# Optimization experiments

Hardware: AMD Instinct MI355X
Metric: run time of the kernel (lower is better)

Reference implementation:

```python
import jax, jax.numpy as jnp
import numpy as np

N, H, W = 128, 64, 64
CH_I, CH_H, CH_Q = 2, 150, 10
N_ACT = 8


def conv3x3(x, w):
    # x: [N,H,W,Cin], w: [3,3,Cin,Cout], 'same' padding, stride 1
    return jax.lax.conv_general_dilated(
        x, w, window_strides=(1, 1), padding='SAME',
        dimension_numbers=('NHWC', 'HWIO', 'NHWC'))


def setup_inputs() -> dict:
    key = jax.random.key(0)
    ks = jax.random.split(key, 9)
    std = 0.01
    x = jax.random.normal(ks[0], (N, H, W, CH_I), dtype=jnp.float32)
    S1 = jax.random.randint(ks[1], (N,), 0, H, dtype=jnp.int32)
    S2 = jax.random.randint(ks[2], (N,), 0, W, dtype=jnp.int32)
    w0 = std * jax.random.normal(ks[3], (3, 3, CH_I, CH_H), dtype=jnp.float32)
    b0 = jnp.zeros((CH_H,), dtype=jnp.float32)
    w_r = std * jax.random.normal(ks[4], (3, 3, CH_H, 1), dtype=jnp.float32)
    w_q = std * jax.random.normal(ks[5], (3, 3, 2, CH_Q), dtype=jnp.float32)
    w_sw = std * jax.random.normal(ks[6], (3, 3, 2, CH_Q), dtype=jnp.float32)
    w_sw2 = std * jax.random.normal(ks[7], (3, 3, 2, CH_Q), dtype=jnp.float32)
    w_dense = std * jax.random.normal(ks[8], (CH_Q, N_ACT), dtype=jnp.float32)
    return {"x": x, "S1": S1, "S2": S2, "VInum": 36,
            "w0": w0, "b0": b0, "w_r": w_r, "w_q": w_q,
            "w_sw": w_sw, "w_sw2": w_sw2, "w_dense": w_dense}


def reference(x, S1, S2, VInum, w0, b0, w_r, w_q, w_sw, w_sw2, w_dense):
    k = int(VInum)
    h = conv3x3(x, w0) + b0                      # [N,H,W,ch_h]
    r = conv3x3(h, w_r)                          # [N,H,W,1] reward map
    v = jnp.zeros_like(r)
    # first VI step uses conv2 weights
    q = conv3x3(jnp.concatenate([r, v], axis=3), w_q)
    v = jnp.max(q, axis=3, keepdims=True)
    # k-1 shared-weight value-iteration steps
    def body(v, _):
        q = conv3x3(jnp.concatenate([r, v], axis=3), w_sw)
        return jnp.max(q, axis=3, keepdims=True), None
    v, _ = jax.lax.scan(body, v, None, length=k - 1)
    # final step with second shared-weight conv
    q = conv3x3(jnp.concatenate([r, v], axis=3), w_sw2)  # [N,H,W,ch_q]
    # attention: gather Q values at state (S1,S2) per batch element
    q_out = q[jnp.arange(q.shape[0]), S1, S2]            # [N,ch_q]
    logits = q_out @ w_dense                             # [N,8]
    prob_actions = jax.nn.softmax(logits, axis=-1)
    return (logits, prob_actions, q, q_out)
```

## Files before the change

### kernel.cpp

```cpp
#include <hip/hip_runtime.h>
#include <math.h>


typedef float v2f __attribute__((ext_vector_type(2)));

static __device__ __forceinline__ v2f splat2(float s) { v2f r; r.x = s; r.y = s; return r; }
static __device__ __forceinline__ v2f pkfma(v2f w, float v, v2f a) {
#if __has_builtin(__builtin_elementwise_fma)
    return __builtin_elementwise_fma(w, splat2(v), a);
#else
    v2f r; r.x = fmaf(w.x, v, a.x); r.y = fmaf(w.y, v, a.y); return r;
#endif
}
static __device__ __forceinline__ v2f pkmax(v2f a, v2f b) {
#if __has_builtin(__builtin_elementwise_max)
    return __builtin_elementwise_max(a, b);
#else
    v2f r; r.x = fmaxf(a.x, b.x); r.y = fmaxf(a.y, b.y); return r;
#endif
}

#define XROW 69
#define VROW 67
#define VSTR (66 * VROW)

__global__ void
__attribute__((amdgpu_flat_work_group_size(512, 512)))
__attribute__((amdgpu_waves_per_eu(2, 2)))
vin_kernel(const float* __restrict__ x,
           const int* __restrict__ S1,
           const int* __restrict__ S2,
           const int* __restrict__ VInum,
           const float* __restrict__ w0,
           const float* __restrict__ b0,
           const float* __restrict__ w_r,
           const float* __restrict__ w_q,
           const float* __restrict__ w_sw,
           const float* __restrict__ w_sw2,
           const float* __restrict__ w_dense,
           float* __restrict__ out) {
    const int b = blockIdx.x;
    const int t = threadIdx.x;

    __shared__ float xs0[68 * XROW];
    __shared__ float xs1[68 * XROW];
    __shared__ float rs[66 * VROW];
    __shared__ float vpool[2 * VSTR];
    __shared__ float wtA[1620];
    __shared__ float Pp[450];
    __shared__ float Bt[90];
    __shared__ float Bv[9];
    __shared__ float W5c[459];
    __shared__ v2f   swv2[45];
    __shared__ float qsel[10];

    for (int i = t; i < 68 * XROW; i += 512) { xs0[i] = 0.f; xs1[i] = 0.f; }
    for (int i = t; i < 66 * VROW; i += 512) rs[i] = 0.f;
    for (int i = t; i < 2 * VSTR; i += 512) vpool[i] = 0.f;
    if (t < 450) Pp[t] = 0.f;
    if (t < 45) {
        int d = t / 5, ap = t - d * 5;
        v2f w; w.x = w_sw[d * 20 + 10 + 2 * ap]; w.y = w_sw[d * 20 + 10 + 2 * ap + 1];
        swv2[t] = w;
    }
    __syncthreads();

    const int row = t >> 3;
    const int cb  = (t & 7) << 3;

    {
        const float* xb = x + (size_t)b * 64 * 64 * 2;
        const float4* xp = (const float4*)(xb + (row * 64 + cb) * 2);
        #pragma unroll
        for (int g = 0; g < 4; ++g) {
            float4 v4 = xp[g];
            int px = cb + g * 2;
            xs0[(row + 2) * XROW + px + 2] = v4.x;
            xs1[(row + 2) * XROW + px + 2] = v4.y;
            xs0[(row + 2) * XROW + px + 3] = v4.z;
            xs1[(row + 2) * XROW + px + 3] = v4.w;
        }
    }
    for (int idx = t; idx < 1620; idx += 512) {
        int entry = idx / 10, ch = idx - entry * 10;
        int d = entry / 18, rem = entry % 18;
        int uu = rem >> 1, ci = rem & 1;
        int c0 = ch * 15;
        const float* wr = w_r + d * 150;
        const float* wp = w0 + (uu * 2 + ci) * 150;
        float s = 0.f;
        for (int c = c0; c < c0 + 15; ++c) s += wr[c] * wp[c];
        wtA[idx] = s;
    }
    if (t < 90) {
        int d = t / 10, ch = t - d * 10, c0 = ch * 15;
        float s = 0.f;
        for (int c = c0; c < c0 + 15; ++c) s += w_r[d * 150 + c] * b0[c];
        Bt[t] = s;
    }
    __syncthreads();
    if (t < 162) {
        float s = 0.f;
        #pragma unroll
        for (int i = 0; i < 10; ++i) s += wtA[t * 10 + i];
        int d = t / 18, rem = t % 18;
        int uu = rem >> 1, ci = rem & 1;
        int dy = d / 3 - 1, dx = d % 3 - 1;
        int uy = uu / 3 - 1, ux = uu % 3 - 1;
        int eidx = (dy + uy + 2) * 5 + (dx + ux + 2);
        Pp[d * 50 + eidx * 2 + ci] = s;
    } else if (t >= 256 && t < 265) {
        int d = t - 256;
        float s = 0.f;
        #pragma unroll
        for (int i = 0; i < 10; ++i) s += Bt[d * 10 + i];
        Bv[d] = s;
    }
    __syncthreads();
    if (t < 459) {
        int cls = t / 51, j = t - cls * 51;
        int cy = cls / 3, cx = cls % 3;
        float s = 0.f;
        #pragma unroll
        for (int d = 0; d < 9; ++d) {
            int dy = d / 3 - 1, dx = d % 3 - 1;
            bool ok = (cy == 0 || (cy == 1 ? dy >= 0 : dy <= 0)) &&
                      (cx == 0 || (cx == 1 ? dx >= 0 : dx <= 0));
            if (ok) s += (j < 50) ? Pp[d * 50 + j] : Bv[d];
        }
        W5c[t] = s;
    }
    __syncthreads();

    {
        int cy = (row == 0) ? 1 : (row == 63) ? 2 : 0;
        #pragma unroll
        for (int p = 0; p < 8; ++p) {
            int xx = cb + p;
            int cx = (xx == 0) ? 1 : (xx == 63) ? 2 : 0;
            const float* Wp = &W5c[(cy * 3 + cx) * 51];
            float acc = Wp[50];
            #pragma unroll
            for (int e = 0; e < 25; ++e) {
                int xi = (row + e / 5) * XROW + (xx + e % 5);
                acc = fmaf(xs0[xi], Wp[e * 2], acc);
                acc = fmaf(xs1[xi], Wp[e * 2 + 1], acc);
            }
            rs[(row + 1) * VROW + (xx + 1)] = acc;
        }
    }
    __syncthreads();

    const int K = VInum[0];

    v2f Rsw2[8][5];
    {
        float rwin[3][10];
        #pragma unroll
        for (int i = 0; i < 3; ++i) {
            const float* rp = &rs[(row + i) * VROW + cb];
            #pragma unroll
            for (int j = 0; j < 10; ++j) rwin[i][j] = rp[j];
        }
        float vmax[8];
        #pragma unroll
        for (int a = 0; a < 10; ++a) {
            #pragma unroll
            for (int p = 0; p < 8; ++p) {
                float accR = 0.f, accQ = 0.f;
                #pragma unroll
                for (int d = 0; d < 9; ++d) {
                    float rv = rwin[d / 3][p + d % 3];
                    accR = fmaf(w_sw[d * 20 + a], rv, accR);
                    accQ = fmaf(w_q[d * 20 + a],  rv, accQ);
                }
                if (a & 1) Rsw2[p][a >> 1].y = accR; else Rsw2[p][a >> 1].x = accR;
                vmax[p] = (a == 0) ? accQ : fmaxf(vmax[p], accQ);
            }
        }
        #pragma unroll
        for (int p = 0; p < 8; ++p)
            vpool[0 * VSTR + (row + 1) * VROW + (cb + p + 1)] = vmax[p];
    }
    __syncthreads();

    int cur = 0;
    for (int it = 0; it < K - 1; ++it) {
        const float* vb = &vpool[cur * VSTR + row * VROW + cb];
        float vwin[3][10];
        #pragma unroll
        for (int i = 0; i < 3; ++i)
            #pragma unroll
            for (int j = 0; j < 10; ++j) vwin[i][j] = vb[i * VROW + j];
        int nxt = cur ^ 1;
        v2f vmax2[8];
        #pragma unroll
        for (int ap = 0; ap < 5; ++ap) {
            v2f acc2[8];
            #pragma unroll
            for (int d = 0; d < 9; ++d) {
                v2f w2 = swv2[d * 5 + ap];
                #pragma unroll
                for (int p = 0; p < 8; ++p) {
                    float vv = vwin[d / 3][p + d % 3];
                    acc2[p] = (d == 0) ? pkfma(w2, vv, Rsw2[p][ap])
                                       : pkfma(w2, vv, acc2[p]);
                }
            }
            #pragma unroll
            for (int p = 0; p < 8; ++p)
                vmax2[p] = (ap == 0) ? acc2[p] : pkmax(vmax2[p], acc2[p]);
        }
        #pragma unroll
        for (int p = 0; p < 8; ++p)
            vpool[nxt * VSTR + (row + 1) * VROW + (cb + p + 1)] =
                fmaxf(vmax2[p].x, vmax2[p].y);
        cur = nxt;
        __syncthreads();
    }

    const int s1 = S1[b], s2 = S2[b];
    {
        float rwin[3][10], vwin[3][10];
        #pragma unroll
        for (int i = 0; i < 3; ++i) {
            const float* rp = &rs[(row + i) * VROW + cb];
            const float* vb = &vpool[cur * VSTR + (row + i) * VROW + cb];
            #pragma unroll
            for (int j = 0; j < 10; ++j) { rwin[i][j] = rp[j]; vwin[i][j] = vb[j]; }
        }
        float qv[8][10];
        #pragma unroll
        for (int a = 0; a < 10; ++a) {
            #pragma unroll
            for (int p = 0; p < 8; ++p) {
                float acc = 0.f;
                #pragma unroll
                for (int d = 0; d < 9; ++d) {
                    acc = fmaf(w_sw2[d * 20 + a],      rwin[d / 3][p + d % 3], acc);
                    acc = fmaf(w_sw2[d * 20 + 10 + a], vwin[d / 3][p + d % 3], acc);
                }
                qv[p][a] = acc;
            }
        }
        {
            float4* qp4 = (float4*)(out + 2048 + ((size_t)((b * 64 + row) * 64 + cb)) * 10);
            #pragma unroll
            for (int g = 0; g < 20; ++g)
                qp4[g] = make_float4(qv[(g * 4) / 10][(g * 4) % 10],
                                     qv[(g * 4 + 1) / 10][(g * 4 + 1) % 10],
                                     qv[(g * 4 + 2) / 10][(g * 4 + 2) % 10],
                                     qv[(g * 4 + 3) / 10][(g * 4 + 3) % 10]);
        }
        if (row == s1) {
            #pragma unroll
            for (int p = 0; p < 8; ++p)
                if (s2 == cb + p) {
                    #pragma unroll
                    for (int a = 0; a < 10; ++a) qsel[a] = qv[p][a];
                }
        }
    }
    __syncthreads();

    if (t == 0) {
        float logits[8];
        float m = -1e30f;
        #pragma unroll
        for (int j = 0; j < 8; ++j) {
            float s = 0.f;
            #pragma unroll
            for (int a = 0; a < 10; ++a) s += qsel[a] * w_dense[a * 8 + j];
            logits[j] = s;
            m = fmaxf(m, s);
        }
        float sum = 0.f;
        float e[8];
        #pragma unroll
        for (int j = 0; j < 8; ++j) { e[j] = expf(logits[j] - m); sum += e[j]; }
        float inv = 1.f / sum;
        #pragma unroll
        for (int j = 0; j < 8; ++j) {
            out[b * 8 + j] = logits[j];
            out[1024 + b * 8 + j] = e[j] * inv;
        }
    }
    if (t < 10) out[5244928 + b * 10 + t] = qsel[t];
}

extern "C" void kernel_launch(void* const* d_in, const int* in_sizes, int n_in,
                              void* d_out, int out_size, void* d_ws, size_t ws_size,
                              hipStream_t stream) {
    const float* x      = (const float*)d_in[0];
    const int*   S1     = (const int*)d_in[1];
    const int*   S2     = (const int*)d_in[2];
    const int*   VInum  = (const int*)d_in[3];
    const float* w0     = (const float*)d_in[4];
    const float* b0     = (const float*)d_in[5];
    const float* w_r    = (const float*)d_in[6];
    const float* w_q    = (const float*)d_in[7];
    const float* w_sw   = (const float*)d_in[8];
    const float* w_sw2  = (const float*)d_in[9];
    const float* w_dense= (const float*)d_in[10];
    float* out = (float*)d_out;

    vin_kernel<<<128, 512, 0, stream>>>(x, S1, S2, VInum, w0, b0, w_r, w_q,
                                        w_sw, w_sw2, w_dense, out);
}
```

Before: 197.1 us.

## Double threads per block, 4 pixels per thread, vectorized LDS window loads

Launches 1024 threads per block instead of 512, so each thread now handles 4 pixels rather than 8. This doubles the waves available to hide LDS latency during the serial value-iteration loop. The shared arrays are padded to 68-float rows so the stencil windows can be read with aligned float4 loads, and each thread keeps its own previous v values in registers rather than reloading them. The packed w_sw weights are now read straight from global memory as uniform loads instead of from LDS. The trade-off is more barrier participants per iteration, a tighter per-thread register budget, and more redundant halo loads per output pixel.

After: 176.7 us. -10.4%, faster.

```diff
diff --git a/kernel.cpp b/kernel.cpp
--- a/kernel.cpp
+++ b/kernel.cpp
@@ -21,12 +21,13 @@
 }
 
 #define XROW 69
-#define VROW 67
-#define VSTR (66 * VROW)
+#define RROW 68
+#define VROW2 68
+#define VSTR2 (66 * VROW2)
 
 __global__ void
-__attribute__((amdgpu_flat_work_group_size(512, 512)))
-__attribute__((amdgpu_waves_per_eu(2, 2)))
+__attribute__((amdgpu_flat_work_group_size(1024, 1024)))
+__attribute__((amdgpu_waves_per_eu(4, 4)))
 vin_kernel(const float* __restrict__ x,
            const int* __restrict__ S1,
            const int* __restrict__ S2,
@@ -44,35 +45,29 @@
 
     __shared__ float xs0[68 * XROW];
     __shared__ float xs1[68 * XROW];
-    __shared__ float rs[66 * VROW];
-    __shared__ float vpool[2 * VSTR];
+    __shared__ float rs[66 * RROW];
+    __shared__ float vpool[2 * VSTR2];
     __shared__ float wtA[1620];
     __shared__ float Pp[450];
     __shared__ float Bt[90];
     __shared__ float Bv[9];
     __shared__ float W5c[459];
-    __shared__ v2f   swv2[45];
     __shared__ float qsel[10];
 
-    for (int i = t; i < 68 * XROW; i += 512) { xs0[i] = 0.f; xs1[i] = 0.f; }
-    for (int i = t; i < 66 * VROW; i += 512) rs[i] = 0.f;
-    for (int i = t; i < 2 * VSTR; i += 512) vpool[i] = 0.f;
+    for (int i = t; i < 68 * XROW; i += 1024) { xs0[i] = 0.f; xs1[i] = 0.f; }
+    for (int i = t; i < 66 * RROW; i += 1024) rs[i] = 0.f;
+    for (int i = t; i < 2 * VSTR2; i += 1024) vpool[i] = 0.f;
     if (t < 450) Pp[t] = 0.f;
-    if (t < 45) {
-        int d = t / 5, ap = t - d * 5;
-        v2f w; w.x = w_sw[d * 20 + 10 + 2 * ap]; w.y = w_sw[d * 20 + 10 + 2 * ap + 1];
-        swv2[t] = w;
-    }
-    __syncthreads();
-
-    const int row = t >> 3;
-    const int cb  = (t & 7) << 3;
+    __syncthreads();
+
+    const int row = t >> 4;
+    const int cb  = (t & 15) << 2;
 
     {
         const float* xb = x + (size_t)b * 64 * 64 * 2;
         const float4* xp = (const float4*)(xb + (row * 64 + cb) * 2);
         #pragma unroll
-        for (int g = 0; g < 4; ++g) {
+        for (int g = 0; g < 2; ++g) {
             float4 v4 = xp[g];
             int px = cb + g * 2;
             xs0[(row + 2) * XROW + px + 2] = v4.x;
@@ -81,7 +76,7 @@
             xs1[(row + 2) * XROW + px + 3] = v4.w;
         }
     }
-    for (int idx = t; idx < 1620; idx += 512) {
+    for (int idx = t; idx < 1620; idx += 1024) {
         int entry = idx / 10, ch = idx - entry * 10;
         int d = entry / 18, rem = entry % 18;
         int uu = rem >> 1, ci = rem & 1;
@@ -135,7 +130,7 @@
     {
         int cy = (row == 0) ? 1 : (row == 63) ? 2 : 0;
         #pragma unroll
-        for (int p = 0; p < 8; ++p) {
+        for (int p = 0; p < 4; ++p) {
             int xx = cb + p;
             int cx = (xx == 0) ? 1 : (xx == 63) ? 2 : 0;
             const float* Wp = &W5c[(cy * 3 + cx) * 51];
@@ -146,27 +141,29 @@
                 acc = fmaf(xs0[xi], Wp[e * 2], acc);
                 acc = fmaf(xs1[xi], Wp[e * 2 + 1], acc);
             }
-            rs[(row + 1) * VROW + (xx + 1)] = acc;
+            rs[(row + 1) * RROW + xx + 2] = acc;
         }
     }
     __syncthreads();
 
     const int K = VInum[0];
 
-    v2f Rsw2[8][5];
+    v2f Rsw2[4][5];
+    float vprev[4];
     {
-        float rwin[3][10];
+        float rwin[3][6];
         #pragma unroll
         for (int i = 0; i < 3; ++i) {
-            const float* rp = &rs[(row + i) * VROW + cb];
-            #pragma unroll
-            for (int j = 0; j < 10; ++j) rwin[i][j] = rp[j];
-        }
-        float vmax[8];
+            const float4* rp = (const float4*)&rs[(row + i) * RROW + cb];
+            float4 cA = rp[0], cB = rp[1];
+            rwin[i][0] = cA.y; rwin[i][1] = cA.z; rwin[i][2] = cA.w;
+            rwin[i][3] = cB.x; rwin[i][4] = cB.y; rwin[i][5] = cB.z;
+        }
+        float vmax[4];
         #pragma unroll
         for (int a = 0; a < 10; ++a) {
             #pragma unroll
-            for (int p = 0; p < 8; ++p) {
+            for (int p = 0; p < 4; ++p) {
                 float accR = 0.f, accQ = 0.f;
                 #pragma unroll
                 for (int d = 0; d < 9; ++d) {
@@ -179,61 +176,96 @@
             }
         }
         #pragma unroll
-        for (int p = 0; p < 8; ++p)
-            vpool[0 * VSTR + (row + 1) * VROW + (cb + p + 1)] = vmax[p];
+        for (int p = 0; p < 4; ++p) {
+            vpool[0 * VSTR2 + (row + 1) * VROW2 + cb + p + 2] = vmax[p];
+            vprev[p] = vmax[p];
+        }
     }
     __syncthreads();
 
     int cur = 0;
     for (int it = 0; it < K - 1; ++it) {
-        const float* vb = &vpool[cur * VSTR + row * VROW + cb];
-        float vwin[3][10];
-        #pragma unroll
-        for (int i = 0; i < 3; ++i)
-            #pragma unroll
-            for (int j = 0; j < 10; ++j) vwin[i][j] = vb[i * VROW + j];
+        const float* vb = &vpool[cur * VSTR2 + row * VROW2 + cb];
+        const float4* r0p = (const float4*)vb;
+        const float4* r2p = (const float4*)(vb + 2 * VROW2);
+        float4 a0 = r0p[0], b0v = r0p[1];
+        float4 a2 = r2p[0], b2v = r2p[1];
+        float eL = vb[VROW2 + 1];
+        float eR = vb[VROW2 + 6];
+        float v0[6], v1[6], v2a[6];
+        v0[0] = a0.y; v0[1] = a0.z; v0[2] = a0.w;
+        v0[3] = b0v.x; v0[4] = b0v.y; v0[5] = b0v.z;
+        v2a[0] = a2.y; v2a[1] = a2.z; v2a[2] = a2.w;
+        v2a[3] = b2v.x; v2a[4] = b2v.y; v2a[5] = b2v.z;
+        v1[0] = eL; v1[5] = eR;
+        #pragma unroll
+        for (int j = 0; j < 4; ++j) v1[j + 1] = vprev[j];
+
         int nxt = cur ^ 1;
-        v2f vmax2[8];
+        v2f vmax2[4];
         #pragma unroll
         for (int ap = 0; ap < 5; ++ap) {
-            v2f acc2[8];
+            v2f acc[4];
             #pragma unroll
             for (int d = 0; d < 9; ++d) {
-                v2f w2 = swv2[d * 5 + ap];
+                v2f w2;
+                w2.x = w_sw[d * 20 + 10 + 2 * ap];
+                w2.y = w_sw[d * 20 + 10 + 2 * ap + 1];
+                const float* vr = (d < 3) ? v0 : (d < 6) ? v1 : v2a;
                 #pragma unroll
-                for (int p = 0; p < 8; ++p) {
-                    float vv = vwin[d / 3][p + d % 3];
-                    acc2[p] = (d == 0) ? pkfma(w2, vv, Rsw2[p][ap])
-                                       : pkfma(w2, vv, acc2[p]);
+                for (int p = 0; p < 4; ++p) {
+                    float vv = vr[p + d % 3];
+                    acc[p] = (d == 0) ? pkfma(w2, vv, Rsw2[p][ap])
+                                      : pkfma(w2, vv, acc[p]);
                 }
             }
             #pragma unroll
-            for (int p = 0; p < 8; ++p)
-                vmax2[p] = (ap == 0) ? acc2[p] : pkmax(vmax2[p], acc2[p]);
-        }
-        #pragma unroll
-        for (int p = 0; p < 8; ++p)
-            vpool[nxt * VSTR + (row + 1) * VROW + (cb + p + 1)] =
-                fmaxf(vmax2[p].x, vmax2[p].y);
+            for (int p = 0; p < 4; ++p)
+                vmax2[p] = (ap == 0) ? acc[p] : pkmax(vmax2[p], acc[p]);
+        }
+        float vnew[4];
+        #pragma unroll
+        for (int p = 0; p < 4; ++p) vnew[p] = fmaxf(vmax2[p].x, vmax2[p].y);
+
+        float* vw = &vpool[nxt * VSTR2 + (row + 1) * VROW2 + cb + 2];
+        *(float2*)&vw[0] = make_float2(vnew[0], vnew[1]);
+        *(float2*)&vw[2] = make_float2(vnew[2], vnew[3]);
+        #pragma unroll
+        for (int p = 0; p < 4; ++p) vprev[p] = vnew[p];
+
         cur = nxt;
         __syncthreads();
     }
 
     const int s1 = S1[b], s2 = S2[b];
     {
-        float rwin[3][10], vwin[3][10];
+        float rwin[3][6], vwin[3][6];
         #pragma unroll
         for (int i = 0; i < 3; ++i) {
-            const float* rp = &rs[(row + i) * VROW + cb];
-            const float* vb = &vpool[cur * VSTR + (row + i) * VROW + cb];
-            #pragma unroll
-            for (int j = 0; j < 10; ++j) { rwin[i][j] = rp[j]; vwin[i][j] = vb[j]; }
-        }
-        float qv[8][10];
+            const float4* rp = (const float4*)&rs[(row + i) * RROW + cb];
+            float4 cA = rp[0], cB = rp[1];
+            rwin[i][0] = cA.y; rwin[i][1] = cA.z; rwin[i][2] = cA.w;
+            rwin[i][3] = cB.x; rwin[i][4] = cB.y; rwin[i][5] = cB.z;
+        }
+        const float* vb = &vpool[cur * VSTR2 + row * VROW2 + cb];
+        {
+            const float4* r0p = (const float4*)vb;
+            const float4* r2p = (const float4*)(vb + 2 * VROW2);
+            float4 a0 = r0p[0], b0v = r0p[1];
+            float4 a2 = r2p[0], b2v = r2p[1];
+            vwin[0][0] = a0.y; vwin[0][1] = a0.z; vwin[0][2] = a0.w;
+            vwin[0][3] = b0v.x; vwin[0][4] = b0v.y; vwin[0][5] = b0v.z;
+            vwin[2][0] = a2.y; vwin[2][1] = a2.z; vwin[2][2] = a2.w;
+            vwin[2][3] = b2v.x; vwin[2][4] = b2v.y; vwin[2][5] = b2v.z;
+            vwin[1][0] = vb[VROW2 + 1]; vwin[1][5] = vb[VROW2 + 6];
+            #pragma unroll
+            for (int j = 0; j < 4; ++j) vwin[1][j + 1] = vprev[j];
+        }
+        float qv[4][10];
         #pragma unroll
         for (int a = 0; a < 10; ++a) {
             #pragma unroll
-            for (int p = 0; p < 8; ++p) {
+            for (int p = 0; p < 4; ++p) {
                 float acc = 0.f;
                 #pragma unroll
                 for (int d = 0; d < 9; ++d) {
@@ -246,7 +278,7 @@
         {
             float4* qp4 = (float4*)(out + 2048 + ((size_t)((b * 64 + row) * 64 + cb)) * 10);
             #pragma unroll
-            for (int g = 0; g < 20; ++g)
+            for (int g = 0; g < 10; ++g)
                 qp4[g] = make_float4(qv[(g * 4) / 10][(g * 4) % 10],
                                      qv[(g * 4 + 1) / 10][(g * 4 + 1) % 10],
                                      qv[(g * 4 + 2) / 10][(g * 4 + 2) % 10],
@@ -254,7 +286,7 @@
         }
         if (row == s1) {
             #pragma unroll
-            for (int p = 0; p < 8; ++p)
+            for (int p = 0; p < 4; ++p)
                 if (s2 == cb + p) {
                     #pragma unroll
                     for (int a = 0; a < 10; ++a) qsel[a] = qv[p][a];
@@ -304,6 +336,6 @@
     const float* w_dense= (const float*)d_in[10];
     float* out = (float*)d_out;
 
-    vin_kernel<<<128, 512, 0, stream>>>(x, S1, S2, VInum, w0, b0, w_r, w_q,
-                                        w_sw, w_sw2, w_dense, out);
+    vin_kernel<<<128, 1024, 0, stream>>>(x, S1, S2, VInum, w0, b0, w_r, w_q,
+                                         w_sw, w_sw2, w_dense, out);
 }
```
